# Performance work log

Hardware: AMD Instinct MI355X
Metric: run time of the kernel (lower is better)

The kernel has to match this reference:

```python
import jax, jax.numpy as jnp
import numpy as np

VOL_MIN = np.array([-40.0, -40.0, -1.0], dtype=np.float32)
VOL_MAX = np.array([40.0, 40.0, 5.4], dtype=np.float32)
VOXEL = 0.4
GRID = (200, 200, 16)          # (vol_max - vol_min) / voxel_size
SIGMA_FACTOR = 3.0
EPS = 1e-6
RMAX = 3                        # max radius given scales <= 0.4: ceil(0.4*3/0.4)=3
N_GAUSS = 16384
FEAT_DIM = 17


def setup_inputs() -> dict:
    key = jax.random.key(0)
    k1, k2, k3, k4, k5 = jax.random.split(key, 5)
    means3d = jnp.asarray(VOL_MIN) + jax.random.uniform(k1, (N_GAUSS, 3)) * jnp.asarray(VOL_MAX - VOL_MIN)
    opacities = jax.random.uniform(k2, (N_GAUSS, 1))
    scales = 0.05 + 0.35 * jax.random.uniform(k3, (N_GAUSS, 3))
    rotations = jax.random.normal(k4, (N_GAUSS, 4))
    features = jax.random.normal(k5, (N_GAUSS, FEAT_DIM))
    return {"means3d": means3d, "opacities": opacities, "scales": scales,
            "rotations": rotations, "features": features}


def _quat_to_rotmat(q):
    # q normalized; torch unbind order: r, x, y, z
    r, x, y, z = q[:, 0], q[:, 1], q[:, 2], q[:, 3]
    R = jnp.stack([
        jnp.stack([1 - 2 * (y * y + z * z), 2 * (x * y - r * z), 2 * (x * z + r * y)], -1),
        jnp.stack([2 * (x * y + r * z), 1 - 2 * (x * x + z * z), 2 * (y * z - r * x)], -1),
        jnp.stack([2 * (x * z - r * y), 2 * (y * z + r * x), 1 - 2 * (x * x + y * y)], -1),
    ], axis=1)  # [N,3,3]
    return R


def reference(means3d, opacities, scales, rotations, features):
    vol_min = jnp.asarray(VOL_MIN)
    grid = jnp.asarray(GRID, dtype=jnp.int32)

    # --- precision matrix (GaussianFormer style) ---
    q = rotations / jnp.sqrt(jnp.sum(rotations ** 2, -1, keepdims=True) + 1e-8)
    R = _quat_to_rotmat(q)
    M = scales[:, :, None] * R                       # S @ R (row-scaled)
    Cov = jnp.einsum('nki,nkj->nij', M, M)           # M^T @ M
    CovInv = jnp.linalg.inv(Cov)                     # [N,3,3]
    cxx, cyy, czz = CovInv[:, 0, 0], CovInv[:, 1, 1], CovInv[:, 2, 2]
    cxy, cyz, cxz = CovInv[:, 0, 1], CovInv[:, 1, 2], CovInv[:, 0, 2]

    radii = jnp.clip(jnp.ceil(scales.max(-1) * SIGMA_FACTOR / VOXEL), 1).astype(jnp.int32)  # [N]

    # --- fixed-window splat with per-gaussian radius mask ---
    mean_idx = jnp.floor((means3d - vol_min) / VOXEL).astype(jnp.int32)  # [N,3]
    off1 = jnp.arange(-RMAX, RMAX + 1, dtype=jnp.int32)
    oi, oj, ok = jnp.meshgrid(off1, off1, off1, indexing='ij')
    offsets = jnp.stack([oi, oj, ok], -1).reshape(-1, 3)                 # [W3,3], W3=343

    idx = mean_idx[:, None, :] + offsets[None, :, :]                     # [N,W3,3]
    centers = idx.astype(jnp.float32) * VOXEL + vol_min + 0.5 * VOXEL
    diff = means3d[:, None, :] - centers                                 # [N,W3,3]
    dx, dy, dz = diff[..., 0], diff[..., 1], diff[..., 2]
    power = (-0.5 * (cxx[:, None] * dx * dx + cyy[:, None] * dy * dy + czz[:, None] * dz * dz)
             - (cxy[:, None] * dx * dy + cyz[:, None] * dy * dz + cxz[:, None] * dx * dz))
    contrib = opacities[:, 0][:, None] * jnp.exp(power)                  # [N,W3]

    in_radius = (jnp.abs(offsets)[None, :, :] <= radii[:, None, None]).all(-1)
    in_grid = ((idx >= 0) & (idx < grid[None, None, :])).all(-1)
    contrib = jnp.where(in_radius & in_grid, contrib, 0.0)

    idx_c = jnp.clip(idx, 0, grid[None, None, :] - 1)
    flat = (idx_c[..., 0] * (GRID[1] * GRID[2]) + idx_c[..., 1] * GRID[2] + idx_c[..., 2]).reshape(-1)
    nvox = GRID[0] * GRID[1] * GRID[2]

    density = jnp.zeros((nvox,), jnp.float32).at[flat].add(contrib.reshape(-1))
    feat_contrib = (contrib[..., None] * features[:, None, :]).reshape(-1, FEAT_DIM)
    feat_acc = jnp.zeros((nvox, FEAT_DIM), jnp.float32).at[flat].add(feat_contrib)

    grid_density = density.reshape(*GRID, 1)
    grid_feats = feat_acc.reshape(*GRID, FEAT_DIM) / jnp.clip(grid_density, EPS)
    return grid_density, grid_feats
```

## Files before the change

### kernel.cpp

```cpp
#include <hip/hip_runtime.h>

#define FEAT_DIM 17
#define GX 200
#define GY 200
#define GZ 16
#define NVOX (GX * GY * GZ)
#define VOXEL 0.4f
#define EPS 1e-6f

#define TS 4
#define NTX (GX / TS)
#define NTY (GY / TS)
#define NTZ (GZ / TS)
#define NTILE (NTX * NTY * NTZ)
#define CAP 96


__global__ __launch_bounds__(256) void prep_kernel(
    const float* __restrict__ means3d,
    const float* __restrict__ opacities,
    const float* __restrict__ scales,
    const float* __restrict__ rotations,
    const float* __restrict__ features,
    float4* __restrict__ P,
    int* __restrict__ cnt,
    unsigned short* __restrict__ list,
    int N)
{
    const int g = blockIdx.x * blockDim.x + threadIdx.x;
    if (g >= N) return;

    const float mx = means3d[g * 3 + 0];
    const float my = means3d[g * 3 + 1];
    const float mz = means3d[g * 3 + 2];
    const float op = opacities[g];
    const float sx = scales[g * 3 + 0];
    const float sy = scales[g * 3 + 1];
    const float sz = scales[g * 3 + 2];
    float qr = rotations[g * 4 + 0];
    float qx = rotations[g * 4 + 1];
    float qy = rotations[g * 4 + 2];
    float qz = rotations[g * 4 + 3];

    const float qinv = 1.0f / sqrtf(qr * qr + qx * qx + qy * qy + qz * qz + 1e-8f);
    qr *= qinv; qx *= qinv; qy *= qinv; qz *= qinv;

    const float R00 = 1.0f - 2.0f * (qy * qy + qz * qz);
    const float R01 = 2.0f * (qx * qy - qr * qz);
    const float R02 = 2.0f * (qx * qz + qr * qy);
    const float R10 = 2.0f * (qx * qy + qr * qz);
    const float R11 = 1.0f - 2.0f * (qx * qx + qz * qz);
    const float R12 = 2.0f * (qy * qz - qr * qx);
    const float R20 = 2.0f * (qx * qz - qr * qy);
    const float R21 = 2.0f * (qy * qz + qr * qx);
    const float R22 = 1.0f - 2.0f * (qx * qx + qy * qy);

    const float M00 = sx * R00, M01 = sx * R01, M02 = sx * R02;
    const float M10 = sy * R10, M11 = sy * R11, M12 = sy * R12;
    const float M20 = sz * R20, M21 = sz * R21, M22 = sz * R22;

    const float C00 = M00 * M00 + M10 * M10 + M20 * M20;
    const float C01 = M00 * M01 + M10 * M11 + M20 * M21;
    const float C02 = M00 * M02 + M10 * M12 + M20 * M22;
    const float C11 = M01 * M01 + M11 * M11 + M21 * M21;
    const float C12 = M01 * M02 + M11 * M12 + M21 * M22;
    const float C22 = M02 * M02 + M12 * M12 + M22 * M22;

    const float a00 = C11 * C22 - C12 * C12;
    const float a01 = C02 * C12 - C01 * C22;
    const float a02 = C01 * C12 - C02 * C11;
    const float det = C00 * a00 + C01 * a01 + C02 * a02;
    const float idet = 1.0f / det;
    const float cxx = a00 * idet;
    const float cxy = a01 * idet;
    const float cxz = a02 * idet;
    const float cyy = (C00 * C22 - C02 * C02) * idet;
    const float cyz = (C01 * C02 - C00 * C12) * idet;
    const float czz = (C00 * C11 - C01 * C01) * idet;

    const float smax = fmaxf(sx, fmaxf(sy, sz));
    int r = (int)ceilf(smax * (3.0f / VOXEL));
    if (r < 1) r = 1;
    if (r > 3) r = 3;

    const int cx = (int)floorf((mx + 40.0f) / VOXEL);
    const int cy = (int)floorf((my + 40.0f) / VOXEL);
    const int cz = (int)floorf((mz + 1.0f) / VOXEL);

    const int pk = (cx & 255) | ((cy & 255) << 8) | ((cz & 63) << 16) | (r << 22);

    float4* p = P + (size_t)g * 7;
    const float* ft = features + (size_t)g * FEAT_DIM;
    p[0] = make_float4(mx, my, mz, op);
    p[1] = make_float4(cxx, cyy, czz, __int_as_float(pk));
    p[2] = make_float4(cxy, cyz, cxz, ft[16]);
    p[3] = make_float4(ft[0], ft[1], ft[2], ft[3]);
    p[4] = make_float4(ft[4], ft[5], ft[6], ft[7]);
    p[5] = make_float4(ft[8], ft[9], ft[10], ft[11]);
    p[6] = make_float4(ft[12], ft[13], ft[14], ft[15]);

    const int txl = max(0, cx - r) / TS, txh = min(GX - 1, cx + r) / TS;
    const int tyl = max(0, cy - r) / TS, tyh = min(GY - 1, cy + r) / TS;
    const int tzl = max(0, cz - r) / TS, tzh = min(GZ - 1, cz + r) / TS;
    for (int tx = txl; tx <= txh; ++tx)
        for (int ty = tyl; ty <= tyh; ++ty)
            for (int tz = tzl; tz <= tzh; ++tz) {
                const int t = (tx * NTY + ty) * NTZ + tz;
                const int pos = atomicAdd(&cnt[t], 1);
                if (pos < CAP) list[(size_t)t * CAP + pos] = (unsigned short)g;
            }
}

__global__ __launch_bounds__(256) void gather_kernel(
    const float4* __restrict__ P,
    const int* __restrict__ cnt,
    const unsigned short* __restrict__ list,
    float* __restrict__ out)
{
    const int wid = threadIdx.x >> 6;
    const int lane = threadIdx.x & 63;
    const int t = blockIdx.x * 4 + wid;

    const int tz = t & (NTZ - 1);
    const int ty = (t >> 2) % NTY;
    const int tx = (t >> 2) / NTY;

    const int lz = lane & 3;
    const int ly = (lane >> 2) & 3;
    const int lx = lane >> 4;
    const int ix = tx * TS + lx;
    const int iy = ty * TS + ly;
    const int iz = tz * TS + lz;

    const float vx = (float)ix * VOXEL - 40.0f + 0.5f * VOXEL;
    const float vy = (float)iy * VOXEL - 40.0f + 0.5f * VOXEL;
    const float vz = (float)iz * VOXEL - 1.0f + 0.5f * VOXEL;

    const int st = __builtin_amdgcn_readfirstlane(t);
    const int ncand = min(cnt[st], CAP);
    const unsigned short* lst = list + (size_t)st * CAP;

    float dacc = 0.0f;
    float facc[FEAT_DIM];
#pragma unroll
    for (int f = 0; f < FEAT_DIM; ++f) facc[f] = 0.0f;

    for (int c = 0; c < ncand; ++c) {
        const int sg = __builtin_amdgcn_readfirstlane((int)lst[c]);
        const float4* p = P + (size_t)sg * 7;
        const float4 p0 = p[0];
        const float4 p1 = p[1];
        const float4 p2 = p[2];
        const float4 f0 = p[3];
        const float4 f1 = p[4];
        const float4 f2 = p[5];
        const float4 f3 = p[6];

        const int pk = __float_as_int(p1.w);
        const int cx = pk & 255;
        const int cy = (pk >> 8) & 255;
        const int cz = (pk >> 16) & 63;
        const int r  = (pk >> 22) & 3;

        const bool inr = (abs(ix - cx) <= r) && (abs(iy - cy) <= r) && (abs(iz - cz) <= r);

        const float dx = p0.x - vx;
        const float dy = p0.y - vy;
        const float dz = p0.z - vz;
        const float power = -0.5f * (p1.x * dx * dx + p1.y * dy * dy + p1.z * dz * dz)
                            - (p2.x * dx * dy + p2.y * dy * dz + p2.z * dx * dz);
        const float w = inr ? p0.w * __expf(power) : 0.0f;

        dacc += w;
        facc[0]  += w * f0.x;  facc[1]  += w * f0.y;
        facc[2]  += w * f0.z;  facc[3]  += w * f0.w;
        facc[4]  += w * f1.x;  facc[5]  += w * f1.y;
        facc[6]  += w * f1.z;  facc[7]  += w * f1.w;
        facc[8]  += w * f2.x;  facc[9]  += w * f2.y;
        facc[10] += w * f2.z;  facc[11] += w * f2.w;
        facc[12] += w * f3.x;  facc[13] += w * f3.y;
        facc[14] += w * f3.z;  facc[16] += w * p2.w;
        facc[15] += w * f3.w;
    }

    const int flat = ix * (GY * GZ) + iy * GZ + iz;
    out[flat] = dacc;

    const float inv = 1.0f / fmaxf(dacc, EPS);
    float* fo = out + NVOX + (size_t)flat * FEAT_DIM;
#pragma unroll
    for (int f = 0; f < FEAT_DIM; ++f) fo[f] = facc[f] * inv;
}

extern "C" void kernel_launch(void* const* d_in, const int* in_sizes, int n_in,
                              void* d_out, int out_size, void* d_ws, size_t ws_size,
                              hipStream_t stream) {
    const float* means3d   = (const float*)d_in[0];
    const float* opacities = (const float*)d_in[1];
    const float* scales    = (const float*)d_in[2];
    const float* rotations = (const float*)d_in[3];
    const float* features  = (const float*)d_in[4];

    const int n_gauss = in_sizes[0] / 3;

    char* ws = (char*)d_ws;
    float4* P = (float4*)ws;
    size_t off = (size_t)n_gauss * 7 * sizeof(float4);
    int* cnt = (int*)(ws + off);
    off += (size_t)NTILE * sizeof(int);
    unsigned short* list = (unsigned short*)(ws + off);

    hipMemsetAsync(cnt, 0, (size_t)NTILE * sizeof(int), stream);

    prep_kernel<<<dim3((n_gauss + 255) / 256), dim3(256), 0, stream>>>(
        means3d, opacities, scales, rotations, features, P, cnt, list, n_gauss);

    gather_kernel<<<dim3(NTILE / 4), dim3(256), 0, stream>>>(P, cnt, list, (float*)d_out);
}
```

Before: 128.1 us.

## Store full gaussian records per tile bin and prefetch next record in gather

```diff
diff --git a/kernel.cpp b/kernel.cpp
--- a/kernel.cpp
+++ b/kernel.cpp
@@ -13,7 +13,7 @@
 #define NTY (GY / TS)
 #define NTZ (GZ / TS)
 #define NTILE (NTX * NTY * NTZ)
-#define CAP 96
+#define CAP 80
 
 
 __global__ __launch_bounds__(256) void prep_kernel(
@@ -22,9 +22,8 @@
     const float* __restrict__ scales,
     const float* __restrict__ rotations,
     const float* __restrict__ features,
-    float4* __restrict__ P,
+    float4* __restrict__ rec,
     int* __restrict__ cnt,
-    unsigned short* __restrict__ list,
     int N)
 {
     const int g = blockIdx.x * blockDim.x + threadIdx.x;
@@ -89,15 +88,14 @@
 
     const int pk = (cx & 255) | ((cy & 255) << 8) | ((cz & 63) << 16) | (r << 22);
 
-    float4* p = P + (size_t)g * 7;
     const float* ft = features + (size_t)g * FEAT_DIM;
-    p[0] = make_float4(mx, my, mz, op);
-    p[1] = make_float4(cxx, cyy, czz, __int_as_float(pk));
-    p[2] = make_float4(cxy, cyz, cxz, ft[16]);
-    p[3] = make_float4(ft[0], ft[1], ft[2], ft[3]);
-    p[4] = make_float4(ft[4], ft[5], ft[6], ft[7]);
-    p[5] = make_float4(ft[8], ft[9], ft[10], ft[11]);
-    p[6] = make_float4(ft[12], ft[13], ft[14], ft[15]);
+    const float4 q0 = make_float4(mx, my, mz, op);
+    const float4 q1 = make_float4(cxx, cyy, czz, __int_as_float(pk));
+    const float4 q2 = make_float4(cxy, cyz, cxz, ft[16]);
+    const float4 q3 = make_float4(ft[0], ft[1], ft[2], ft[3]);
+    const float4 q4 = make_float4(ft[4], ft[5], ft[6], ft[7]);
+    const float4 q5 = make_float4(ft[8], ft[9], ft[10], ft[11]);
+    const float4 q6 = make_float4(ft[12], ft[13], ft[14], ft[15]);
 
     const int txl = max(0, cx - r) / TS, txh = min(GX - 1, cx + r) / TS;
     const int tyl = max(0, cy - r) / TS, tyh = min(GY - 1, cy + r) / TS;
@@ -107,14 +105,17 @@
             for (int tz = tzl; tz <= tzh; ++tz) {
                 const int t = (tx * NTY + ty) * NTZ + tz;
                 const int pos = atomicAdd(&cnt[t], 1);
-                if (pos < CAP) list[(size_t)t * CAP + pos] = (unsigned short)g;
+                if (pos < CAP) {
+                    float4* dst = rec + ((size_t)t * CAP + pos) * 7;
+                    dst[0] = q0; dst[1] = q1; dst[2] = q2; dst[3] = q3;
+                    dst[4] = q4; dst[5] = q5; dst[6] = q6;
+                }
             }
 }
 
 __global__ __launch_bounds__(256) void gather_kernel(
-    const float4* __restrict__ P,
+    const float4* __restrict__ rec,
     const int* __restrict__ cnt,
-    const unsigned short* __restrict__ list,
     float* __restrict__ out)
 {
     const int wid = threadIdx.x >> 6;
@@ -138,49 +139,49 @@
 
     const int st = __builtin_amdgcn_readfirstlane(t);
     const int ncand = min(cnt[st], CAP);
-    const unsigned short* lst = list + (size_t)st * CAP;
+    const float4* base = rec + (size_t)st * CAP * 7;
 
     float dacc = 0.0f;
     float facc[FEAT_DIM];
 #pragma unroll
     for (int f = 0; f < FEAT_DIM; ++f) facc[f] = 0.0f;
 
-    for (int c = 0; c < ncand; ++c) {
-        const int sg = __builtin_amdgcn_readfirstlane((int)lst[c]);
-        const float4* p = P + (size_t)sg * 7;
-        const float4 p0 = p[0];
-        const float4 p1 = p[1];
-        const float4 p2 = p[2];
-        const float4 f0 = p[3];
-        const float4 f1 = p[4];
-        const float4 f2 = p[5];
-        const float4 f3 = p[6];
-
-        const int pk = __float_as_int(p1.w);
-        const int cx = pk & 255;
-        const int cy = (pk >> 8) & 255;
-        const int cz = (pk >> 16) & 63;
-        const int r  = (pk >> 22) & 3;
-
-        const bool inr = (abs(ix - cx) <= r) && (abs(iy - cy) <= r) && (abs(iz - cz) <= r);
-
-        const float dx = p0.x - vx;
-        const float dy = p0.y - vy;
-        const float dz = p0.z - vz;
-        const float power = -0.5f * (p1.x * dx * dx + p1.y * dy * dy + p1.z * dz * dz)
-                            - (p2.x * dx * dy + p2.y * dy * dz + p2.z * dx * dz);
-        const float w = inr ? p0.w * __expf(power) : 0.0f;
-
-        dacc += w;
-        facc[0]  += w * f0.x;  facc[1]  += w * f0.y;
-        facc[2]  += w * f0.z;  facc[3]  += w * f0.w;
-        facc[4]  += w * f1.x;  facc[5]  += w * f1.y;
-        facc[6]  += w * f1.z;  facc[7]  += w * f1.w;
-        facc[8]  += w * f2.x;  facc[9]  += w * f2.y;
-        facc[10] += w * f2.z;  facc[11] += w * f2.w;
-        facc[12] += w * f3.x;  facc[13] += w * f3.y;
-        facc[14] += w * f3.z;  facc[16] += w * p2.w;
-        facc[15] += w * f3.w;
+    if (ncand > 0) {
+        float4 a0 = base[0], a1 = base[1], a2 = base[2], a3 = base[3],
+               a4 = base[4], a5 = base[5], a6 = base[6];
+        for (int c = 0; c < ncand; ++c) {
+            const int cn = min(c + 1, ncand - 1);
+            const float4* nb = base + (size_t)cn * 7;
+            const float4 b0 = nb[0], b1 = nb[1], b2 = nb[2], b3 = nb[3],
+                         b4 = nb[4], b5 = nb[5], b6 = nb[6];
+
+            const int pk = __float_as_int(a1.w);
+            const int cx = pk & 255;
+            const int cy = (pk >> 8) & 255;
+            const int cz = (pk >> 16) & 63;
+            const int r  = (pk >> 22) & 3;
+            const bool inr = (abs(ix - cx) <= r) && (abs(iy - cy) <= r) && (abs(iz - cz) <= r);
+
+            const float dx = a0.x - vx;
+            const float dy = a0.y - vy;
+            const float dz = a0.z - vz;
+            const float power = -0.5f * (a1.x * dx * dx + a1.y * dy * dy + a1.z * dz * dz)
+                                - (a2.x * dx * dy + a2.y * dy * dz + a2.z * dx * dz);
+            const float w = inr ? a0.w * __expf(power) : 0.0f;
+
+            dacc += w;
+            facc[0]  += w * a3.x;  facc[1]  += w * a3.y;
+            facc[2]  += w * a3.z;  facc[3]  += w * a3.w;
+            facc[4]  += w * a4.x;  facc[5]  += w * a4.y;
+            facc[6]  += w * a4.z;  facc[7]  += w * a4.w;
+            facc[8]  += w * a5.x;  facc[9]  += w * a5.y;
+            facc[10] += w * a5.z;  facc[11] += w * a5.w;
+            facc[12] += w * a6.x;  facc[13] += w * a6.y;
+            facc[14] += w * a6.z;  facc[15] += w * a6.w;
+            facc[16] += w * a2.w;
+
+            a0 = b0; a1 = b1; a2 = b2; a3 = b3; a4 = b4; a5 = b5; a6 = b6;
+        }
     }
 
     const int flat = ix * (GY * GZ) + iy * GZ + iz;
@@ -204,16 +205,13 @@
     const int n_gauss = in_sizes[0] / 3;
 
     char* ws = (char*)d_ws;
-    float4* P = (float4*)ws;
-    size_t off = (size_t)n_gauss * 7 * sizeof(float4);
-    int* cnt = (int*)(ws + off);
-    off += (size_t)NTILE * sizeof(int);
-    unsigned short* list = (unsigned short*)(ws + off);
+    float4* rec = (float4*)ws;
+    int* cnt = (int*)(ws + (size_t)NTILE * CAP * 7 * sizeof(float4));
 
     hipMemsetAsync(cnt, 0, (size_t)NTILE * sizeof(int), stream);
 
     prep_kernel<<<dim3((n_gauss + 255) / 256), dim3(256), 0, stream>>>(
-        means3d, opacities, scales, rotations, features, P, cnt, list, n_gauss);
-
-    gather_kernel<<<dim3(NTILE / 4), dim3(256), 0, stream>>>(P, cnt, list, (float*)d_out);
+        means3d, opacities, scales, rotations, features, rec, cnt, n_gauss);
+
+    gather_kernel<<<dim3(NTILE / 4), dim3(256), 0, stream>>>(rec, cnt, (float*)d_out);
 }
```

Result: slower. 141.4 us (+10.4%).
